# Kernel optimization log

Measured on AMD Instinct MI355X. Metric: run time of the kernel, lower is better.

Reference implementation:

```python
import jax, jax.numpy as jnp
import numpy as np

S, D = 4096, 64
DROPOUT_P = 0.1


def setup_inputs() -> dict:
    key = jax.random.key(0)
    k1, k2, k3, k4, k5, k6 = jax.random.split(key, 6)
    return {
        "query": jax.random.normal(k1, (S, D), dtype=jnp.float32),
        "key": jax.random.normal(k2, (S, D), dtype=jnp.float32),
        "value": jax.random.normal(k3, (S, D), dtype=jnp.float32),
        "u_drop": jax.random.uniform(k4, (S, S), dtype=jnp.float32),
        "row_rand": jax.random.uniform(k5, (S, 1), dtype=jnp.float32),
        "x": jax.random.normal(k6, (1,), dtype=jnp.float32),
    }


def reference(query, key, value, u_drop, row_rand, x):
    d = query.shape[-1]
    # torch code divides by scale_factor = d**-0.5, i.e. multiplies by sqrt(d)
    qk = jnp.matmul(query, key.T) * jnp.asarray(d, query.dtype) ** 0.5  # [S,S]
    # dropout with keep prob (1-p), inverted scaling (matches F.dropout)
    keep = (u_drop >= DROPOUT_P).astype(qk.dtype) / (1.0 - DROPOUT_P)
    t = qk * keep  # [S,S]
    # drop_rows_or_cols: random floor mask normalized by its global sum
    r = jnp.floor(t * row_rand)          # [S,S] (row_rand broadcasts over cols)
    t = t * (r / jnp.sum(r))             # [S,S]
    return jnp.matmul(t, value)          # [S,D]
```

## Files before the change

### kernel.cpp

```cpp
#include <hip/hip_runtime.h>
#include <stdint.h>


#define S 4096
#define D 64
#define NCHUNK 8
#define JCHUNK (S / NCHUNK)
#define JT 128
#define NTILES (JCHUNK / JT)
#define KSCALE (8.0f / 0.9f)

typedef float f32x4 __attribute__((ext_vector_type(4)));
typedef short s16x8 __attribute__((ext_vector_type(8)));
typedef unsigned short u16x4 __attribute__((ext_vector_type(4)));
typedef int i32x4 __attribute__((ext_vector_type(4)));
typedef const __attribute__((address_space(1))) unsigned g_u32;
typedef __attribute__((address_space(3))) unsigned lds_u32;

__device__ inline unsigned short f2bf(float f) {
    union { float f; unsigned u; } v; v.f = f;
    unsigned r = v.u + 0x7fffu + ((v.u >> 16) & 1u);
    return (unsigned short)(r >> 16);
}

__device__ inline unsigned cvt_pk_bf16(float lo, float hi) {
    unsigned r;
    asm("v_cvt_pk_bf16_f32 %0, %1, %2" : "=v"(r) : "v"(lo), "v"(hi));
    return r;
}

__global__ void prep_all(const float* __restrict__ Q,
                         const float* __restrict__ Kf,
                         const float* __restrict__ V,
                         short* __restrict__ Qbf, short* __restrict__ Kbf,
                         short* __restrict__ VTbf, int* __restrict__ sumr) {
    __shared__ short tile[64 * 68];
    const int b   = blockIdx.x;
    const int tid = threadIdx.x;
    if (b == 0 && tid == 0) *sumr = 0;

    if (b < 512) {
        const int idx = b * 256 + tid;
        if (idx < 65536) {
            float4 v = ((const float4*)Q)[idx];
            u16x4 o; o[0] = f2bf(v.x); o[1] = f2bf(v.y); o[2] = f2bf(v.z); o[3] = f2bf(v.w);
            ((u16x4*)Qbf)[idx] = o;
        } else {
            const int k = idx - 65536;
            float4 v = ((const float4*)Kf)[k];
            u16x4 o; o[0] = f2bf(v.x * KSCALE); o[1] = f2bf(v.y * KSCALE);
                     o[2] = f2bf(v.z * KSCALE); o[3] = f2bf(v.w * KSCALE);
            ((u16x4*)Kbf)[k] = o;
        }
    } else {
        const int j0 = (b - 512) * 64;
#pragma unroll
        for (int it = 0; it < 4; ++it) {
            const int f4 = tid + it * 256;
            const int row = f4 >> 4, c4 = (f4 & 15) * 4;
            float4 v = *(const float4*)&V[(size_t)(j0 + row) * D + c4];
            tile[(c4 + 0) * 68 + row] = (short)f2bf(v.x);
            tile[(c4 + 1) * 68 + row] = (short)f2bf(v.y);
            tile[(c4 + 2) * 68 + row] = (short)f2bf(v.z);
            tile[(c4 + 3) * 68 + row] = (short)f2bf(v.w);
        }
        __syncthreads();
#pragma unroll
        for (int it = 0; it < 4; ++it) {
            const int f4 = tid + it * 256;
            const int d = f4 >> 4, o4 = (f4 & 15) * 4;
            u16x4 w = *(const u16x4*)&tile[d * 68 + o4];
            *(u16x4*)&VTbf[(size_t)d * S + j0 + o4] = w;
        }
    }
}

__launch_bounds__(256, 2)
__global__ void fused_main(const short* __restrict__ Qbf,
                           const short* __restrict__ Kbf,
                           const short* __restrict__ VTbf,
                           const float* __restrict__ Ud,
                           const float* __restrict__ RR,
                           float* __restrict__ Opart,
                           int* __restrict__ sumr)
{
    __shared__ short kb[2][16 * 512];
    __shared__ short vb[2][16 * 512];
    __shared__ int red[4];

    const int tid  = threadIdx.x;
    const int w    = tid >> 6;
    const int lane = tid & 63;
    const int quad = lane >> 4;
    const int n16  = lane & 15;

    const int ib  = blockIdx.x & 63;
    const int ic  = blockIdx.x >> 6;
    const int i0w = ib * 64 + w * 16;
    const int jbase = ic * JCHUNK;

    const float* uln = Ud + (size_t)(i0w + n16) * S + quad * 4;

    s16x8 aQ[2];
#pragma unroll
    for (int ks = 0; ks < 2; ++ks)
        aQ[ks] = *(const s16x8*)&Qbf[(size_t)(i0w + n16) * D + ks * 32 + quad * 8];

    const float rrn = RR[i0w + n16];

    f32x4 accO[4];
#pragma unroll
    for (int ds = 0; ds < 4; ++ds) accO[ds] = (f32x4){0.f, 0.f, 0.f, 0.f};

    float lsum = 0.f;
    float4 un[8];
    unsigned um;

    {
#pragma unroll
        for (int p = 0; p < 4; ++p) {
            const int e = w * 4 + p;
            __builtin_amdgcn_global_load_lds(
                (g_u32*)&Kbf[(size_t)(jbase + (e >> 1) * 16 + n16) * D + (e & 1) * 32 + quad * 8],
                (lds_u32*)&kb[0][e * 512], 16, 0, 0);
        }
#pragma unroll
        for (int p = 0; p < 4; ++p) {
            const int e = w * 4 + p;
            __builtin_amdgcn_global_load_lds(
                (g_u32*)&VTbf[(size_t)((e & 3) * 16 + n16) * S + jbase + (e >> 2) * 32 + quad * 8],
                (lds_u32*)&vb[0][e * 512], 16, 0, 0);
        }
#pragma unroll
        for (int c = 0; c < 8; ++c)
            un[c] = *(const float4*)&uln[jbase + c * 16];
        __asm__ volatile("s_waitcnt vmcnt(8)" ::: "memory");
        __builtin_amdgcn_s_barrier();
        __asm__ volatile("" ::: "memory");
    }

#pragma unroll
    for (int jt = 0; jt < NTILES; ++jt) {
        const int bu = jt & 1;
        const int nb = bu ^ 1;
        const bool last = (jt + 1 == NTILES);

        if (!last) {
            const int j1 = jbase + (jt + 1) * JT;
#pragma unroll
            for (int p = 0; p < 4; ++p) {
                const int e = w * 4 + p;
                __builtin_amdgcn_global_load_lds(
                    (g_u32*)&Kbf[(size_t)(j1 + (e >> 1) * 16 + n16) * D + (e & 1) * 32 + quad * 8],
                    (lds_u32*)&kb[nb][e * 512], 16, 0, 0);
            }
#pragma unroll
            for (int p = 0; p < 4; ++p) {
                const int e = w * 4 + p;
                __builtin_amdgcn_global_load_lds(
                    (g_u32*)&VTbf[(size_t)((e & 3) * 16 + n16) * S + j1 + (e >> 2) * 32 + quad * 8],
                    (lds_u32*)&vb[nb][e * 512], 16, 0, 0);
            }
        }

        {
            unsigned m = 0;
#pragma unroll
            for (int c = 0; c < 8; ++c) {
                m |= (un[c].x >= 0.1f ? 1u : 0u) << (c * 4 + 0);
                m |= (un[c].y >= 0.1f ? 1u : 0u) << (c * 4 + 1);
                m |= (un[c].z >= 0.1f ? 1u : 0u) << (c * 4 + 2);
                m |= (un[c].w >= 0.1f ? 1u : 0u) << (c * 4 + 3);
            }
            um = m;
        }
        if (!last) {
            const int j1 = jbase + (jt + 1) * JT;
#pragma unroll
            for (int c = 0; c < 8; ++c)
                un[c] = *(const float4*)&uln[j1 + c * 16];
        }

        unsigned pkw[16];
#pragma unroll
        for (int cs = 0; cs < 8; ++cs) {
            f32x4 acc = (f32x4){0.f, 0.f, 0.f, 0.f};
#pragma unroll
            for (int ks = 0; ks < 2; ++ks) {
                s16x8 bK = *(const s16x8*)&kb[bu][(cs * 2 + ks) * 512 + lane * 8];
                acc = __builtin_amdgcn_mfma_f32_16x16x32_bf16(bK, aQ[ks], acc, 0, 0, 0);
            }
            float vv[4];
#pragma unroll
            for (int rg = 0; rg < 4; ++rg) {
                const float t = ((um >> (cs * 4 + rg)) & 1u) ? acc[rg] : 0.0f;
                const float r = floorf(t * rrn);
                lsum += r;
                vv[rg] = t * r;
            }
            pkw[cs * 2]     = cvt_pk_bf16(vv[0], vv[1]);
            pkw[cs * 2 + 1] = cvt_pk_bf16(vv[2], vv[3]);
        }

        const int pbase = (32 * ((lane >> 4) & 1) + n16) * 4;
#pragma unroll
        for (int ksj = 0; ksj < 4; ++ksj) {
            i32x4 aw;
#pragma unroll
            for (int widx = 0; widx < 4; ++widx) {
                const int addr = pbase + (widx >> 1) * 64;
                const int lo = __builtin_amdgcn_ds_bpermute(addr, (int)pkw[ksj * 4 + (widx & 1)]);
                const int hi = __builtin_amdgcn_ds_bpermute(addr, (int)pkw[ksj * 4 + 2 + (widx & 1)]);
                aw[widx] = (lane >= 32) ? hi : lo;
            }
            s16x8 aP;
            __builtin_memcpy(&aP, &aw, 16);
#pragma unroll
            for (int ds = 0; ds < 4; ++ds) {
                s16x8 bV = *(const s16x8*)&vb[bu][(ksj * 4 + ds) * 512 + lane * 8];
                accO[ds] = __builtin_amdgcn_mfma_f32_16x16x32_bf16(aP, bV, accO[ds], 0, 0, 0);
            }
        }

        if (!last) {
            __asm__ volatile("s_waitcnt vmcnt(8)" ::: "memory");
            __builtin_amdgcn_s_barrier();
            __asm__ volatile("" ::: "memory");
        }
    }

    float* op = Opart + (size_t)ic * S * D;
#pragma unroll
    for (int ds = 0; ds < 4; ++ds) {
        const int d = ds * 16 + n16;
#pragma unroll
        for (int rg = 0; rg < 4; ++rg) {
            const int i = i0w + quad * 4 + rg;
            op[(size_t)i * D + d] = accO[ds][rg];
        }
    }

    for (int off = 32; off; off >>= 1) lsum += __shfl_down(lsum, off);
    if (lane == 0) red[w] = (int)lsum;
    __syncthreads();
    if (tid == 0) atomicAdd(sumr, red[0] + red[1] + red[2] + red[3]);
}

__global__ void reduce_out(const float* __restrict__ Opart,
                           const int* __restrict__ sumr,
                           float* __restrict__ out) {
    const int idx = blockIdx.x * 256 + threadIdx.x;
    const float invR = 1.0f / (float)(*sumr);
    float sx = 0.f, sy = 0.f, sz = 0.f, sw = 0.f;
#pragma unroll
    for (int c = 0; c < NCHUNK; ++c) {
        const float4 v = ((const float4*)(Opart + (size_t)c * S * D))[idx];
        sx += v.x; sy += v.y; sz += v.z; sw += v.w;
    }
    float4 o; o.x = sx * invR; o.y = sy * invR; o.z = sz * invR; o.w = sw * invR;
    ((float4*)out)[idx] = o;
}

extern "C" void kernel_launch(void* const* d_in, const int* in_sizes, int n_in,
                              void* d_out, int out_size, void* d_ws, size_t ws_size,
                              hipStream_t stream) {
    (void)in_sizes; (void)n_in; (void)out_size; (void)ws_size;
    const float* Q  = (const float*)d_in[0];
    const float* Kf = (const float*)d_in[1];
    const float* V  = (const float*)d_in[2];
    const float* Ud = (const float*)d_in[3];
    const float* RR = (const float*)d_in[4];
    float* out = (float*)d_out;

    char* ws = (char*)d_ws;
    float* Opart = (float*)ws;
    short* Qbf  = (short*)(ws + (8u << 20));
    short* Kbf  = (short*)(ws + (8u << 20) + (512u << 10));
    short* VTbf = (short*)(ws + (8u << 20) + (1024u << 10));
    int*   sumr = (int*)  (ws + (8u << 20) + (1536u << 10));

    prep_all<<<dim3(576), dim3(256), 0, stream>>>(Q, Kf, V, Qbf, Kbf, VTbf, sumr);
    fused_main<<<dim3(64 * NCHUNK), dim3(256), 0, stream>>>(
        Qbf, Kbf, VTbf, Ud, RR, Opart, sumr);
    reduce_out<<<dim3(256), dim3(256), 0, stream>>>(Opart, sumr, out);
}
```

Baseline: 120.9 us.

## Convert Q in-kernel and fold split-K reduction into last-arriving block

```diff
diff --git a/kernel.cpp b/kernel.cpp
--- a/kernel.cpp
+++ b/kernel.cpp
@@ -1,5 +1,4 @@
 #include <hip/hip_runtime.h>
-#include <stdint.h>
 
 
 #define S 4096
@@ -29,31 +28,27 @@
     return r;
 }
 
-__global__ void prep_all(const float* __restrict__ Q,
-                         const float* __restrict__ Kf,
+__global__ void prep_all(const float* __restrict__ Kf,
                          const float* __restrict__ V,
-                         short* __restrict__ Qbf, short* __restrict__ Kbf,
-                         short* __restrict__ VTbf, int* __restrict__ sumr) {
+                         short* __restrict__ Kbf,
+                         short* __restrict__ VTbf,
+                         int* __restrict__ sumr, int* __restrict__ cnt) {
     __shared__ short tile[64 * 68];
     const int b   = blockIdx.x;
     const int tid = threadIdx.x;
-    if (b == 0 && tid == 0) *sumr = 0;
-
-    if (b < 512) {
-        const int idx = b * 256 + tid;
-        if (idx < 65536) {
-            float4 v = ((const float4*)Q)[idx];
-            u16x4 o; o[0] = f2bf(v.x); o[1] = f2bf(v.y); o[2] = f2bf(v.z); o[3] = f2bf(v.w);
-            ((u16x4*)Qbf)[idx] = o;
-        } else {
-            const int k = idx - 65536;
-            float4 v = ((const float4*)Kf)[k];
-            u16x4 o; o[0] = f2bf(v.x * KSCALE); o[1] = f2bf(v.y * KSCALE);
-                     o[2] = f2bf(v.z * KSCALE); o[3] = f2bf(v.w * KSCALE);
-            ((u16x4*)Kbf)[k] = o;
-        }
+    if (b == 0) {
+        if (tid == 0) *sumr = 0;
+        if (tid < 64) cnt[tid] = 0;
+    }
+
+    if (b < 256) {
+        const int k = b * 256 + tid;
+        float4 v = ((const float4*)Kf)[k];
+        u16x4 o; o[0] = f2bf(v.x * KSCALE); o[1] = f2bf(v.y * KSCALE);
+                 o[2] = f2bf(v.z * KSCALE); o[3] = f2bf(v.w * KSCALE);
+        ((u16x4*)Kbf)[k] = o;
     } else {
-        const int j0 = (b - 512) * 64;
+        const int j0 = (b - 256) * 64;
 #pragma unroll
         for (int it = 0; it < 4; ++it) {
             const int f4 = tid + it * 256;
@@ -76,13 +71,15 @@
 }
 
 __launch_bounds__(256, 2)
-__global__ void fused_main(const short* __restrict__ Qbf,
+__global__ void fused_main(const float* __restrict__ Qf,
                            const short* __restrict__ Kbf,
                            const short* __restrict__ VTbf,
                            const float* __restrict__ Ud,
                            const float* __restrict__ RR,
                            float* __restrict__ Opart,
-                           int* __restrict__ sumr)
+                           float* __restrict__ out,
+                           int* __restrict__ sumr,
+                           int* __restrict__ cnt)
 {
     __shared__ short kb[2][16 * 512];
     __shared__ short vb[2][16 * 512];
@@ -103,8 +100,17 @@
 
     s16x8 aQ[2];
 #pragma unroll
-    for (int ks = 0; ks < 2; ++ks)
-        aQ[ks] = *(const s16x8*)&Qbf[(size_t)(i0w + n16) * D + ks * 32 + quad * 8];
+    for (int ks = 0; ks < 2; ++ks) {
+        const float* qp = &Qf[(size_t)(i0w + n16) * D + ks * 32 + quad * 8];
+        f32x4 qa = *(const f32x4*)qp;
+        f32x4 qb = *(const f32x4*)(qp + 4);
+        i32x4 aw;
+        aw[0] = (int)cvt_pk_bf16(qa[0], qa[1]);
+        aw[1] = (int)cvt_pk_bf16(qa[2], qa[3]);
+        aw[2] = (int)cvt_pk_bf16(qb[0], qb[1]);
+        aw[3] = (int)cvt_pk_bf16(qb[2], qb[3]);
+        __builtin_memcpy(&aQ[ks], &aw, 16);
+    }
 
     const float rrn = RR[i0w + n16];
 
@@ -239,26 +245,42 @@
             op[(size_t)i * D + d] = accO[ds][rg];
         }
     }
+    __threadfence();
 
     for (int off = 32; off; off >>= 1) lsum += __shfl_down(lsum, off);
     if (lane == 0) red[w] = (int)lsum;
     __syncthreads();
-    if (tid == 0) atomicAdd(sumr, red[0] + red[1] + red[2] + red[3]);
-}
-
-__global__ void reduce_out(const float* __restrict__ Opart,
-                           const int* __restrict__ sumr,
-                           float* __restrict__ out) {
+    if (tid == 0) {
+        atomicAdd(sumr, red[0] + red[1] + red[2] + red[3]);
+        red[0] = atomicAdd(&cnt[ib], 1);
+    }
+    __syncthreads();
+
+    if (red[0] == NCHUNK - 1) {
+        __threadfence();
+        const size_t base = (size_t)ib * 64 * D;
+#pragma unroll
+        for (int k = 0; k < 4; ++k) {
+            const int o = tid + k * 256;
+            float sx = 0.f, sy = 0.f, sz = 0.f, sw = 0.f;
+#pragma unroll
+            for (int c = 0; c < NCHUNK; ++c) {
+                const float4 v = ((const float4*)(Opart + (size_t)c * S * D + base))[o];
+                sx += v.x; sy += v.y; sz += v.z; sw += v.w;
+            }
+            float4 s; s.x = sx; s.y = sy; s.z = sz; s.w = sw;
+            ((float4*)(out + base))[o] = s;
+        }
+    }
+}
+
+__global__ void scale_out(const int* __restrict__ sumr,
+                          float* __restrict__ out) {
     const int idx = blockIdx.x * 256 + threadIdx.x;
     const float invR = 1.0f / (float)(*sumr);
-    float sx = 0.f, sy = 0.f, sz = 0.f, sw = 0.f;
-#pragma unroll
-    for (int c = 0; c < NCHUNK; ++c) {
-        const float4 v = ((const float4*)(Opart + (size_t)c * S * D))[idx];
-        sx += v.x; sy += v.y; sz += v.z; sw += v.w;
-    }
-    float4 o; o.x = sx * invR; o.y = sy * invR; o.z = sz * invR; o.w = sw * invR;
-    ((float4*)out)[idx] = o;
+    float4 v = ((const float4*)out)[idx];
+    v.x *= invR; v.y *= invR; v.z *= invR; v.w *= invR;
+    ((float4*)out)[idx] = v;
 }
 
 extern "C" void kernel_launch(void* const* d_in, const int* in_sizes, int n_in,
@@ -274,13 +296,13 @@
 
     char* ws = (char*)d_ws;
     float* Opart = (float*)ws;
-    short* Qbf  = (short*)(ws + (8u << 20));
-    short* Kbf  = (short*)(ws + (8u << 20) + (512u << 10));
-    short* VTbf = (short*)(ws + (8u << 20) + (1024u << 10));
-    int*   sumr = (int*)  (ws + (8u << 20) + (1536u << 10));
-
-    prep_all<<<dim3(576), dim3(256), 0, stream>>>(Q, Kf, V, Qbf, Kbf, VTbf, sumr);
+    short* Kbf  = (short*)(ws + (8u << 20));
+    short* VTbf = (short*)(ws + (8u << 20) + (512u << 10));
+    int*   sumr = (int*)  (ws + (8u << 20) + (1024u << 10));
+    int*   cnt  = (int*)  (ws + (8u << 20) + (1024u << 10) + 256);
+
+    prep_all<<<dim3(320), dim3(256), 0, stream>>>(Kf, V, Kbf, VTbf, sumr, cnt);
     fused_main<<<dim3(64 * NCHUNK), dim3(256), 0, stream>>>(
-        Qbf, Kbf, VTbf, Ud, RR, Opart, sumr);
-    reduce_out<<<dim3(256), dim3(256), 0, stream>>>(Opart, sumr, out);
-}
+        Q, Kbf, VTbf, Ud, RR, Opart, out, sumr, cnt);
+    scale_out<<<dim3(256), dim3(256), 0, stream>>>(sumr, out);
+}
```

New measurement: 202.3 us. 1.67x slower.

## Split key range into 16 chunks with 64-wide tiles and convert Q in-kernel

Applied to the files above, without the earlier changes.

```diff
diff --git a/kernel.cpp b/kernel.cpp
--- a/kernel.cpp
+++ b/kernel.cpp
@@ -1,12 +1,11 @@
 #include <hip/hip_runtime.h>
-#include <stdint.h>
 
 
 #define S 4096
 #define D 64
-#define NCHUNK 8
+#define NCHUNK 16
 #define JCHUNK (S / NCHUNK)
-#define JT 128
+#define JT 64
 #define NTILES (JCHUNK / JT)
 #define KSCALE (8.0f / 0.9f)
 
@@ -29,31 +28,24 @@
     return r;
 }
 
-__global__ void prep_all(const float* __restrict__ Q,
-                         const float* __restrict__ Kf,
+__global__ void prep_all(const float* __restrict__ Kf,
                          const float* __restrict__ V,
-                         short* __restrict__ Qbf, short* __restrict__ Kbf,
-                         short* __restrict__ VTbf, int* __restrict__ sumr) {
+                         short* __restrict__ Kbf,
+                         short* __restrict__ VTbf,
+                         int* __restrict__ sumr) {
     __shared__ short tile[64 * 68];
     const int b   = blockIdx.x;
     const int tid = threadIdx.x;
     if (b == 0 && tid == 0) *sumr = 0;
 
-    if (b < 512) {
-        const int idx = b * 256 + tid;
-        if (idx < 65536) {
-            float4 v = ((const float4*)Q)[idx];
-            u16x4 o; o[0] = f2bf(v.x); o[1] = f2bf(v.y); o[2] = f2bf(v.z); o[3] = f2bf(v.w);
-            ((u16x4*)Qbf)[idx] = o;
-        } else {
-            const int k = idx - 65536;
-            float4 v = ((const float4*)Kf)[k];
-            u16x4 o; o[0] = f2bf(v.x * KSCALE); o[1] = f2bf(v.y * KSCALE);
-                     o[2] = f2bf(v.z * KSCALE); o[3] = f2bf(v.w * KSCALE);
-            ((u16x4*)Kbf)[k] = o;
-        }
+    if (b < 256) {
+        const int k = b * 256 + tid;
+        float4 v = ((const float4*)Kf)[k];
+        u16x4 o; o[0] = f2bf(v.x * KSCALE); o[1] = f2bf(v.y * KSCALE);
+                 o[2] = f2bf(v.z * KSCALE); o[3] = f2bf(v.w * KSCALE);
+        ((u16x4*)Kbf)[k] = o;
     } else {
-        const int j0 = (b - 512) * 64;
+        const int j0 = (b - 256) * 64;
 #pragma unroll
         for (int it = 0; it < 4; ++it) {
             const int f4 = tid + it * 256;
@@ -75,8 +67,8 @@
     }
 }
 
-__launch_bounds__(256, 2)
-__global__ void fused_main(const short* __restrict__ Qbf,
+__launch_bounds__(256, 4)
+__global__ void fused_main(const float* __restrict__ Qf,
                            const short* __restrict__ Kbf,
                            const short* __restrict__ VTbf,
                            const float* __restrict__ Ud,
@@ -84,8 +76,8 @@
                            float* __restrict__ Opart,
                            int* __restrict__ sumr)
 {
-    __shared__ short kb[2][16 * 512];
-    __shared__ short vb[2][16 * 512];
+    __shared__ short kb[2][8 * 512];
+    __shared__ short vb[2][8 * 512];
     __shared__ int red[4];
 
     const int tid  = threadIdx.x;
@@ -103,8 +95,17 @@
 
     s16x8 aQ[2];
 #pragma unroll
-    for (int ks = 0; ks < 2; ++ks)
-        aQ[ks] = *(const s16x8*)&Qbf[(size_t)(i0w + n16) * D + ks * 32 + quad * 8];
+    for (int ks = 0; ks < 2; ++ks) {
+        const float* qp = &Qf[(size_t)(i0w + n16) * D + ks * 32 + quad * 8];
+        f32x4 qa = *(const f32x4*)qp;
+        f32x4 qb = *(const f32x4*)(qp + 4);
+        i32x4 aw;
+        aw[0] = (int)cvt_pk_bf16(qa[0], qa[1]);
+        aw[1] = (int)cvt_pk_bf16(qa[2], qa[3]);
+        aw[2] = (int)cvt_pk_bf16(qb[0], qb[1]);
+        aw[3] = (int)cvt_pk_bf16(qb[2], qb[3]);
+        __builtin_memcpy(&aQ[ks], &aw, 16);
+    }
 
     const float rrn = RR[i0w + n16];
 
@@ -113,28 +114,28 @@
     for (int ds = 0; ds < 4; ++ds) accO[ds] = (f32x4){0.f, 0.f, 0.f, 0.f};
 
     float lsum = 0.f;
-    float4 un[8];
+    float4 un[4];
     unsigned um;
 
     {
 #pragma unroll
-        for (int p = 0; p < 4; ++p) {
-            const int e = w * 4 + p;
+        for (int p = 0; p < 2; ++p) {
+            const int e = w * 2 + p;
             __builtin_amdgcn_global_load_lds(
                 (g_u32*)&Kbf[(size_t)(jbase + (e >> 1) * 16 + n16) * D + (e & 1) * 32 + quad * 8],
                 (lds_u32*)&kb[0][e * 512], 16, 0, 0);
         }
 #pragma unroll
-        for (int p = 0; p < 4; ++p) {
-            const int e = w * 4 + p;
+        for (int p = 0; p < 2; ++p) {
+            const int e = w * 2 + p;
             __builtin_amdgcn_global_load_lds(
                 (g_u32*)&VTbf[(size_t)((e & 3) * 16 + n16) * S + jbase + (e >> 2) * 32 + quad * 8],
                 (lds_u32*)&vb[0][e * 512], 16, 0, 0);
         }
 #pragma unroll
-        for (int c = 0; c < 8; ++c)
+        for (int c = 0; c < 4; ++c)
             un[c] = *(const float4*)&uln[jbase + c * 16];
-        __asm__ volatile("s_waitcnt vmcnt(8)" ::: "memory");
+        __asm__ volatile("s_waitcnt vmcnt(4)" ::: "memory");
         __builtin_amdgcn_s_barrier();
         __asm__ volatile("" ::: "memory");
     }
@@ -148,15 +149,15 @@
         if (!last) {
             const int j1 = jbase + (jt + 1) * JT;
 #pragma unroll
-            for (int p = 0; p < 4; ++p) {
-                const int e = w * 4 + p;
+            for (int p = 0; p < 2; ++p) {
+                const int e = w * 2 + p;
                 __builtin_amdgcn_global_load_lds(
                     (g_u32*)&Kbf[(size_t)(j1 + (e >> 1) * 16 + n16) * D + (e & 1) * 32 + quad * 8],
                     (lds_u32*)&kb[nb][e * 512], 16, 0, 0);
             }
 #pragma unroll
-            for (int p = 0; p < 4; ++p) {
-                const int e = w * 4 + p;
+            for (int p = 0; p < 2; ++p) {
+                const int e = w * 2 + p;
                 __builtin_amdgcn_global_load_lds(
                     (g_u32*)&VTbf[(size_t)((e & 3) * 16 + n16) * S + j1 + (e >> 2) * 32 + quad * 8],
                     (lds_u32*)&vb[nb][e * 512], 16, 0, 0);
@@ -166,7 +167,7 @@
         {
             unsigned m = 0;
 #pragma unroll
-            for (int c = 0; c < 8; ++c) {
+            for (int c = 0; c < 4; ++c) {
                 m |= (un[c].x >= 0.1f ? 1u : 0u) << (c * 4 + 0);
                 m |= (un[c].y >= 0.1f ? 1u : 0u) << (c * 4 + 1);
                 m |= (un[c].z >= 0.1f ? 1u : 0u) << (c * 4 + 2);
@@ -177,13 +178,13 @@
         if (!last) {
             const int j1 = jbase + (jt + 1) * JT;
 #pragma unroll
-            for (int c = 0; c < 8; ++c)
+            for (int c = 0; c < 4; ++c)
                 un[c] = *(const float4*)&uln[j1 + c * 16];
         }
 
-        unsigned pkw[16];
-#pragma unroll
-        for (int cs = 0; cs < 8; ++cs) {
+        unsigned pkw[8];
+#pragma unroll
+        for (int cs = 0; cs < 4; ++cs) {
             f32x4 acc = (f32x4){0.f, 0.f, 0.f, 0.f};
 #pragma unroll
             for (int ks = 0; ks < 2; ++ks) {
@@ -204,7 +205,7 @@
 
         const int pbase = (32 * ((lane >> 4) & 1) + n16) * 4;
 #pragma unroll
-        for (int ksj = 0; ksj < 4; ++ksj) {
+        for (int ksj = 0; ksj < 2; ++ksj) {
             i32x4 aw;
 #pragma unroll
             for (int widx = 0; widx < 4; ++widx) {
@@ -223,7 +224,7 @@
         }
 
         if (!last) {
-            __asm__ volatile("s_waitcnt vmcnt(8)" ::: "memory");
+            __asm__ volatile("s_waitcnt vmcnt(4)" ::: "memory");
             __builtin_amdgcn_s_barrier();
             __asm__ volatile("" ::: "memory");
         }
@@ -274,13 +275,12 @@
 
     char* ws = (char*)d_ws;
     float* Opart = (float*)ws;
-    short* Qbf  = (short*)(ws + (8u << 20));
-    short* Kbf  = (short*)(ws + (8u << 20) + (512u << 10));
-    short* VTbf = (short*)(ws + (8u << 20) + (1024u << 10));
-    int*   sumr = (int*)  (ws + (8u << 20) + (1536u << 10));
-
-    prep_all<<<dim3(576), dim3(256), 0, stream>>>(Q, Kf, V, Qbf, Kbf, VTbf, sumr);
+    short* Kbf  = (short*)(ws + (16u << 20));
+    short* VTbf = (short*)(ws + (16u << 20) + (512u << 10));
+    int*   sumr = (int*)  (ws + (16u << 20) + (1024u << 10));
+
+    prep_all<<<dim3(320), dim3(256), 0, stream>>>(Kf, V, Kbf, VTbf, sumr);
     fused_main<<<dim3(64 * NCHUNK), dim3(256), 0, stream>>>(
-        Qbf, Kbf, VTbf, Ud, RR, Opart, sumr);
+        Q, Kbf, VTbf, Ud, RR, Opart, sumr);
     reduce_out<<<dim3(256), dim3(256), 0, stream>>>(Opart, sumr, out);
 }
```

New measurement: 126.2 us. 4.4% more time.
